# Kernel optimization log

Hardware: AMD Instinct MI355X
Metric: run time of the kernel (lower is better)

Reference implementation:

```python
import jax, jax.numpy as jnp
import numpy as np

N, E = 50000, 800000
H, C_HID = 4, 64  # heads, hidden_units
C_IN, C_OUT = 256, 64
NEG_SLOPE = 0.2
EPS = 1e-16


def gat_conv(x, src, dst, W, att_src, att_dst, bias):
    """PyG GATConv with concat=False (mean over heads) + bias.
    x: [N, F_in], W: [F_in, H*C], att_*: [H, C], bias: [C]."""
    n = x.shape[0]
    h = (x @ W).reshape(n, H, -1)                     # [N, H, C]
    a_src = jnp.sum(h * att_src, axis=-1)             # [N, H]
    a_dst = jnp.sum(h * att_dst, axis=-1)             # [N, H]
    e = jax.nn.leaky_relu(a_src[src] + a_dst[dst], NEG_SLOPE)  # [E, H]
    # segment softmax grouped by destination node
    m = jax.ops.segment_max(e, dst, num_segments=n)   # [N, H]
    e = jnp.exp(e - m[dst])
    denom = jax.ops.segment_sum(e, dst, num_segments=n)
    alpha = e / (denom[dst] + EPS)                    # [E, H]
    msg = h[src] * alpha[:, :, None]                  # [E, H, C]
    out = jax.ops.segment_sum(msg, dst, num_segments=n)  # [N, H, C]
    return out.mean(axis=1) + bias                    # concat=False -> head mean


def setup_inputs() -> dict:
    key = jax.random.key(0)
    ks = jax.random.split(key, 16)
    inp = {
        "x": jax.random.normal(ks[0], (N, C_IN), dtype=jnp.float32),
        "edge_index": jax.random.randint(ks[1], (2, E), 0, N, dtype=jnp.int64),
    }
    dims = [(C_IN, C_HID), (C_HID, C_HID), (C_HID, C_OUT)]
    for i, (fi, fo) in enumerate(dims, start=1):
        inp[f"W{i}"] = jax.random.normal(ks[2 + 4 * (i - 1)], (fi, H * fo), dtype=jnp.float32) * (1.0 / np.sqrt(fi))
        inp[f"as{i}"] = jax.random.normal(ks[3 + 4 * (i - 1)], (H, fo), dtype=jnp.float32) * 0.1
        inp[f"ad{i}"] = jax.random.normal(ks[4 + 4 * (i - 1)], (H, fo), dtype=jnp.float32) * 0.1
        inp[f"b{i}"] = jnp.zeros((fo,), dtype=jnp.float32)
    return inp


def reference(x, edge_index, W1, as1, ad1, b1, W2, as2, ad2, b2, W3, as3, ad3, b3):
    n = x.shape[0]
    loop = jnp.arange(n, dtype=edge_index.dtype)
    src = jnp.concatenate([edge_index[0], loop])  # add_self_loops=True (PyG default)
    dst = jnp.concatenate([edge_index[1], loop])
    layers = [(W1, as1, ad1, b1), (W2, as2, ad2, b2), (W3, as3, ad3, b3)]
    for (W, a_s, a_d, b) in layers:
        x = gat_conv(x, src, dst, W, a_s, a_d, b)
        x = jax.nn.relu(x)  # dropout is identity at inference
    return jax.nn.log_softmax(x, axis=-1)
```

## Files before the change

### kernel.cpp

```cpp
#include <hip/hip_runtime.h>
#include <hip/hip_bf16.h>
#include <math.h>
#include <stdint.h>

#define HEADS 4
#define CH 64
#define HC 256
#define NEG 0.2f
#define EPSV 1e-16f
#define NEGBIG -3.0e38f

typedef __attribute__((ext_vector_type(8))) short short8;
typedef __attribute__((ext_vector_type(4))) float f32x4;

__device__ __forceinline__ float lrelu(float x) { return x > 0.f ? x : NEG * x; }

__device__ __forceinline__ unsigned short f2bf(float f) {
  __hip_bfloat16 b = __float2bfloat16(f);
  return *reinterpret_cast<unsigned short*>(&b);
}
__device__ __forceinline__ float bf2f(unsigned short u) {
  return __uint_as_float((unsigned)u << 16);
}
__device__ __forceinline__ unsigned int packbf2(float a, float b) {
  return (unsigned int)f2bf(a) | ((unsigned int)f2bf(b) << 16);
}
__device__ __forceinline__ float unpack_lo(unsigned int v) {
  return __uint_as_float(v << 16);
}
__device__ __forceinline__ float unpack_hi(unsigned int v) {
  return __uint_as_float(v & 0xffff0000u);
}

__global__ __launch_bounds__(256) void wprep_k(const float* __restrict__ W,
                                               unsigned short* __restrict__ Wt,
                                               int K) {
  int i = blockIdx.x * 256 + threadIdx.x;
  if (i >= K * 256) return;
  int k = i >> 8, n = i & 255;
  Wt[(size_t)n * K + k] = f2bf(W[i]);
}

__global__ __launch_bounds__(256) void mfma_gat_k(const float* __restrict__ Af,
                                                  const unsigned short* __restrict__ Ab,
                                                  const unsigned short* __restrict__ Wt,
                                                  const float* __restrict__ att_s,
                                                  const float* __restrict__ att_d,
                                                  unsigned short* __restrict__ hb16,
                                                  float* __restrict__ a_src,
                                                  float* __restrict__ a_dst,
                                                  int M, int K, int a_is_f32) {
  __shared__ unsigned short As[32 * 40];
  __shared__ unsigned short Bs[256 * 40];
  __shared__ unsigned short Cs[32 * 258];

  int tid = threadIdx.x;
  int bm = blockIdx.x * 32;
  int w = tid >> 6, l = tid & 63;
  int lr = l & 15, lk = l >> 4;
  int row_s = tid >> 3, seg = tid & 7;

  f32x4 acc[2][4];
  #pragma unroll
  for (int rt = 0; rt < 2; ++rt)
    #pragma unroll
    for (int ct = 0; ct < 4; ++ct) {
      f32x4 z = {0.f, 0.f, 0.f, 0.f};
      acc[rt][ct] = z;
    }

  for (int k0 = 0; k0 < K; k0 += 32) {
    if (a_is_f32) {
      float4 v = make_float4(0.f, 0.f, 0.f, 0.f);
      if (bm + row_s < M)
        v = *reinterpret_cast<const float4*>(Af + (size_t)(bm + row_s) * K + k0 + seg * 4);
      ushort4 u;
      u.x = f2bf(v.x); u.y = f2bf(v.y); u.z = f2bf(v.z); u.w = f2bf(v.w);
      *reinterpret_cast<ushort4*>(&As[row_s * 40 + seg * 4]) = u;
    } else {
      ushort4 u = make_ushort4(0, 0, 0, 0);
      if (bm + row_s < M)
        u = *reinterpret_cast<const ushort4*>(Ab + (size_t)(bm + row_s) * K + k0 + seg * 4);
      *reinterpret_cast<ushort4*>(&As[row_s * 40 + seg * 4]) = u;
    }
    {
      const uint4* srcq = reinterpret_cast<const uint4*>(Wt + (size_t)tid * K + k0);
      uint4 q0 = srcq[0], q1 = srcq[1], q2 = srcq[2], q3 = srcq[3];
      uint4* dstq = reinterpret_cast<uint4*>(&Bs[tid * 40]);
      dstq[0] = q0; dstq[1] = q1; dstq[2] = q2; dstq[3] = q3;
    }
    __syncthreads();
    short8 bfr[4];
    #pragma unroll
    for (int ct = 0; ct < 4; ++ct)
      bfr[ct] = *reinterpret_cast<const short8*>(&Bs[(w * 64 + ct * 16 + lr) * 40 + lk * 8]);
    #pragma unroll
    for (int rt = 0; rt < 2; ++rt) {
      short8 af = *reinterpret_cast<const short8*>(&As[(rt * 16 + lr) * 40 + lk * 8]);
      #pragma unroll
      for (int ct = 0; ct < 4; ++ct)
        acc[rt][ct] = __builtin_amdgcn_mfma_f32_16x16x32_bf16(af, bfr[ct], acc[rt][ct], 0, 0, 0);
    }
    __syncthreads();
  }

  #pragma unroll
  for (int rt = 0; rt < 2; ++rt)
    #pragma unroll
    for (int ct = 0; ct < 4; ++ct)
      #pragma unroll
      for (int r = 0; r < 4; ++r) {
        int row = rt * 16 + lk * 4 + r;
        int c = ct * 16 + lr;
        Cs[row * 258 + c * 4 + w] = f2bf(acc[rt][ct][r]);
      }
  __syncthreads();

  if (bm + row_s < M) {
    ushort4* dst = reinterpret_cast<ushort4*>(hb16 + (size_t)(bm + row_s) * HC + seg * 32);
    const unsigned short* srcp = &Cs[row_s * 258 + seg * 32];
    #pragma unroll
    for (int q = 0; q < 4; ++q)
      dst[q] = *reinterpret_cast<const ushort4*>(srcp + q * 4);
  }

  {
    int nd = tid >> 3, q = tid & 7, h = q >> 1, half = q & 1;
    float ps = 0.f, pd = 0.f;
    const float* ats = att_s + h * 64 + half * 32;
    const float* atd = att_d + h * 64 + half * 32;
    const unsigned short* cp = &Cs[nd * 258 + (half * 32) * 4 + h];
    #pragma unroll
    for (int c = 0; c < 32; ++c) {
      float hv = bf2f(cp[c * 4]);
      ps += hv * ats[c];
      pd += hv * atd[c];
    }
    ps += __shfl_xor(ps, 1);
    pd += __shfl_xor(pd, 1);
    if (!(q & 1) && bm + nd < M) {
      a_src[(size_t)(bm + nd) * 4 + h] = ps;
      a_dst[(size_t)(bm + nd) * 4 + h] = pd;
    }
  }
}

__global__ __launch_bounds__(256) void zero2_k(int* __restrict__ a, int* __restrict__ b, int n) {
  int i = blockIdx.x * blockDim.x + threadIdx.x;
  if (i < n) { a[i] = 0; b[i] = 0; }
}

__global__ __launch_bounds__(256) void hist_k(const int* __restrict__ dst, int* __restrict__ count, int E) {
  int e = blockIdx.x * blockDim.x + threadIdx.x;
  if (e < E) atomicAdd(&count[dst[e]], 1);
}

__global__ __launch_bounds__(512) void scan1_k(const int* __restrict__ count,
                                               int* __restrict__ rp,
                                               int* __restrict__ bsum, int n) {
  __shared__ int sh[512];
  int tx = threadIdx.x;
  int i = blockIdx.x * 512 + tx;
  int v = (i < n) ? count[i] : 0;
  sh[tx] = v;
  __syncthreads();
  #pragma unroll
  for (int off = 1; off < 512; off <<= 1) {
    int t = (tx >= off) ? sh[tx - off] : 0;
    __syncthreads();
    sh[tx] += t;
    __syncthreads();
  }
  if (i < n) rp[i] = sh[tx] - v;
  if (tx == 511) bsum[blockIdx.x] = sh[511];
}

__global__ __launch_bounds__(128) void scan2_k(int* __restrict__ bsum, int nb) {
  __shared__ int sh[128];
  int tx = threadIdx.x;
  int v = (tx < nb) ? bsum[tx] : 0;
  sh[tx] = v;
  __syncthreads();
  #pragma unroll
  for (int off = 1; off < 128; off <<= 1) {
    int t = (tx >= off) ? sh[tx - off] : 0;
    __syncthreads();
    sh[tx] += t;
    __syncthreads();
  }
  if (tx < nb) bsum[tx] = sh[tx] - v;
}

__global__ __launch_bounds__(512) void scan3_k(int* __restrict__ rp, const int* __restrict__ bsum,
                                               int n, int E) {
  int i = blockIdx.x * 512 + threadIdx.x;
  if (i < n) rp[i] += bsum[blockIdx.x];
  if (i == 0) rp[n] = E;
}

__global__ __launch_bounds__(256) void scatter_k(const int* __restrict__ src, const int* __restrict__ dst,
                                                 const int* __restrict__ rp, int* __restrict__ cursor,
                                                 int* __restrict__ csr_src, int E) {
  int e = blockIdx.x * blockDim.x + threadIdx.x;
  if (e >= E) return;
  int d = dst[e];
  int pos = rp[d] + atomicAdd(&cursor[d], 1);
  csr_src[pos] = src[e];
}

__global__ __launch_bounds__(256) void soft_agg_k(const int* __restrict__ rp,
                                                  const int* __restrict__ csr_src,
                                                  const float* __restrict__ a_src,
                                                  const float* __restrict__ a_dst,
                                                  const unsigned short* __restrict__ hb16,
                                                  const float* __restrict__ bias,
                                                  float* __restrict__ outf,
                                                  unsigned short* __restrict__ outb,
                                                  int N, int do_lsm) {
  __shared__ uint4 rec[4][64];
  int tid  = threadIdx.x;
  int w    = tid >> 6;
  int lane = tid & 63;
  int wid  = (blockIdx.x * blockDim.x + tid) >> 6;
  if (wid >= N) return;
  int rs = rp[wid], re = rp[wid + 1];

  float4 ad4 = *reinterpret_cast<const float4*>(a_dst + (size_t)wid * 4);
  float4 asn = *reinterpret_cast<const float4*>(a_src + (size_t)wid * 4);
  float es0 = lrelu(asn.x + ad4.x), es1 = lrelu(asn.y + ad4.y);
  float es2 = lrelu(asn.z + ad4.z), es3 = lrelu(asn.w + ad4.w);

  int sreg = 0;
  float e0 = NEGBIG, e1 = NEGBIG, e2 = NEGBIG, e3 = NEGBIG;
  if (rs + lane < re) {
    sreg = csr_src[rs + lane];
    float4 a = *reinterpret_cast<const float4*>(a_src + (size_t)sreg * 4);
    e0 = lrelu(a.x + ad4.x); e1 = lrelu(a.y + ad4.y);
    e2 = lrelu(a.z + ad4.z); e3 = lrelu(a.w + ad4.w);
  }
  float m0 = fmaxf(es0, e0), m1 = fmaxf(es1, e1);
  float m2 = fmaxf(es2, e2), m3 = fmaxf(es3, e3);
  for (int base = rs + 64; base < re; base += 64) {
    if (base + lane < re) {
      int s = csr_src[base + lane];
      float4 a = *reinterpret_cast<const float4*>(a_src + (size_t)s * 4);
      m0 = fmaxf(m0, lrelu(a.x + ad4.x)); m1 = fmaxf(m1, lrelu(a.y + ad4.y));
      m2 = fmaxf(m2, lrelu(a.z + ad4.z)); m3 = fmaxf(m3, lrelu(a.w + ad4.w));
    }
  }
  #pragma unroll
  for (int off = 32; off > 0; off >>= 1) {
    m0 = fmaxf(m0, __shfl_xor(m0, off));
    m1 = fmaxf(m1, __shfl_xor(m1, off));
    m2 = fmaxf(m2, __shfl_xor(m2, off));
    m3 = fmaxf(m3, __shfl_xor(m3, off));
  }

  float a0 = 0.f, a1 = 0.f, a2 = 0.f, a3 = 0.f;
  float dn0 = 0.f, dn1 = 0.f, dn2 = 0.f, dn3 = 0.f;
  uint4* recw = &rec[w][0];
  const unsigned short* hl = hb16 + lane * 4;

  auto agg_lds = [&](int cnt) {
    int k = 0;
    for (; k + 4 <= cnt; k += 4) {
      uint4 r0 = recw[k + 0], r1 = recw[k + 1], r2 = recw[k + 2], r3 = recw[k + 3];
      ushort4 h0 = *reinterpret_cast<const ushort4*>(hl + (size_t)r0.x * HC);
      ushort4 h1 = *reinterpret_cast<const ushort4*>(hl + (size_t)r1.x * HC);
      ushort4 h2 = *reinterpret_cast<const ushort4*>(hl + (size_t)r2.x * HC);
      ushort4 h3 = *reinterpret_cast<const ushort4*>(hl + (size_t)r3.x * HC);
      a0 += unpack_lo(r0.y) * bf2f(h0.x) + unpack_lo(r1.y) * bf2f(h1.x)
          + unpack_lo(r2.y) * bf2f(h2.x) + unpack_lo(r3.y) * bf2f(h3.x);
      a1 += unpack_hi(r0.y) * bf2f(h0.y) + unpack_hi(r1.y) * bf2f(h1.y)
          + unpack_hi(r2.y) * bf2f(h2.y) + unpack_hi(r3.y) * bf2f(h3.y);
      a2 += unpack_lo(r0.z) * bf2f(h0.z) + unpack_lo(r1.z) * bf2f(h1.z)
          + unpack_lo(r2.z) * bf2f(h2.z) + unpack_lo(r3.z) * bf2f(h3.z);
      a3 += unpack_hi(r0.z) * bf2f(h0.w) + unpack_hi(r1.z) * bf2f(h1.w)
          + unpack_hi(r2.z) * bf2f(h2.w) + unpack_hi(r3.z) * bf2f(h3.w);
    }
    for (; k < cnt; ++k) {
      uint4 r0 = recw[k];
      ushort4 hv = *reinterpret_cast<const ushort4*>(hl + (size_t)r0.x * HC);
      a0 += unpack_lo(r0.y) * bf2f(hv.x);
      a1 += unpack_hi(r0.y) * bf2f(hv.y);
      a2 += unpack_lo(r0.z) * bf2f(hv.z);
      a3 += unpack_hi(r0.z) * bf2f(hv.w);
    }
  };

  {
    float px = expf(e0 - m0), py = expf(e1 - m1);
    float pz = expf(e2 - m2), pw = expf(e3 - m3);
    dn0 += px; dn1 += py; dn2 += pz; dn3 += pw;
    recw[lane] = make_uint4((unsigned)sreg, packbf2(px, py), packbf2(pz, pw), 0u);
    int cnt = re - rs; if (cnt > 64) cnt = 64;
    agg_lds(cnt);
  }
  for (int base = rs + 64; base < re; base += 64) {
    int s = 0;
    float f0 = NEGBIG, f1 = NEGBIG, f2 = NEGBIG, f3 = NEGBIG;
    if (base + lane < re) {
      s = csr_src[base + lane];
      float4 a = *reinterpret_cast<const float4*>(a_src + (size_t)s * 4);
      f0 = lrelu(a.x + ad4.x); f1 = lrelu(a.y + ad4.y);
      f2 = lrelu(a.z + ad4.z); f3 = lrelu(a.w + ad4.w);
    }
    float px = expf(f0 - m0), py = expf(f1 - m1);
    float pz = expf(f2 - m2), pw = expf(f3 - m3);
    dn0 += px; dn1 += py; dn2 += pz; dn3 += pw;
    recw[lane] = make_uint4((unsigned)s, packbf2(px, py), packbf2(pz, pw), 0u);
    int cnt = re - base; if (cnt > 64) cnt = 64;
    agg_lds(cnt);
  }

  #pragma unroll
  for (int off = 32; off > 0; off >>= 1) {
    dn0 += __shfl_xor(dn0, off);
    dn1 += __shfl_xor(dn1, off);
    dn2 += __shfl_xor(dn2, off);
    dn3 += __shfl_xor(dn3, off);
  }
  float sp0 = expf(es0 - m0), sp1 = expf(es1 - m1);
  float sp2 = expf(es2 - m2), sp3 = expf(es3 - m3);
  dn0 += sp0; dn1 += sp1; dn2 += sp2; dn3 += sp3;
  float r0 = 1.f / (dn0 + EPSV), r1 = 1.f / (dn1 + EPSV);
  float r2 = 1.f / (dn2 + EPSV), r3 = 1.f / (dn3 + EPSV);

  ushort4 sh = *reinterpret_cast<const ushort4*>(hb16 + (size_t)wid * HC + lane * 4);
  float sum = (a0 + sp0 * bf2f(sh.x)) * r0
            + (a1 + sp1 * bf2f(sh.y)) * r1
            + (a2 + sp2 * bf2f(sh.z)) * r2
            + (a3 + sp3 * bf2f(sh.w)) * r3;
  float v = sum * 0.25f + bias[lane];
  v = fmaxf(v, 0.f);
  if (do_lsm) {
    float mx = v;
    #pragma unroll
    for (int off = 32; off > 0; off >>= 1) mx = fmaxf(mx, __shfl_xor(mx, off));
    float ex = expf(v - mx);
    float sm = ex;
    #pragma unroll
    for (int off = 32; off > 0; off >>= 1) sm += __shfl_xor(sm, off);
    outf[(size_t)wid * CH + lane] = v - mx - logf(sm);
  } else {
    outb[(size_t)wid * CH + lane] = f2bf(v);
  }
}

extern "C" void kernel_launch(void* const* d_in, const int* in_sizes, int n_in,
                              void* d_out, int out_size, void* d_ws, size_t ws_size,
                              hipStream_t stream) {
  const float* x0 = (const float*)d_in[0];
  const int*   ei = (const int*)d_in[1];
  int N = in_sizes[0] / HC;
  int E = in_sizes[1] / 2;
  const int* srcp = ei;
  const int* dstp = ei + E;

  const float* W[3]  = {(const float*)d_in[2], (const float*)d_in[6],  (const float*)d_in[10]};
  const float* AS[3] = {(const float*)d_in[3], (const float*)d_in[7],  (const float*)d_in[11]};
  const float* AD[3] = {(const float*)d_in[4], (const float*)d_in[8],  (const float*)d_in[12]};
  const float* BI[3] = {(const float*)d_in[5], (const float*)d_in[9],  (const float*)d_in[13]};
  int Kdim[3] = {256, 64, 64};

  char* ws = (char*)d_ws;
  size_t off = 0;
  auto alloc = [&](size_t bytes) {
    void* p = ws + off;
    off += (bytes + 255) & ~(size_t)255;
    return p;
  };
  unsigned short* hb16    = (unsigned short*)alloc((size_t)N * HC * 2);
  unsigned short* xb16    = (unsigned short*)alloc((size_t)N * CH * 2);
  float*          a_s     = (float*)alloc((size_t)N * 4 * 4);
  float*          a_d     = (float*)alloc((size_t)N * 4 * 4);
  int*            rowp    = (int*)alloc((size_t)(N + 1) * 4);
  int*            cursor  = (int*)alloc((size_t)N * 4);
  int*            csr_src = (int*)alloc((size_t)E * 4);
  int*            bsum    = (int*)alloc(512 * 4);
  unsigned short* Wt[3];
  Wt[0] = (unsigned short*)alloc((size_t)256 * 256 * 2);
  Wt[1] = (unsigned short*)alloc((size_t)256 * 64 * 2);
  Wt[2] = (unsigned short*)alloc((size_t)256 * 64 * 2);

  for (int L = 0; L < 3; ++L) {
    int tot = Kdim[L] * 256;
    wprep_k<<<(tot + 255) / 256, 256, 0, stream>>>(W[L], Wt[L], Kdim[L]);
  }

  int nb = (N + 511) / 512;
  zero2_k<<<(N + 255) / 256, 256, 0, stream>>>(cursor, rowp, N);
  hist_k<<<(E + 255) / 256, 256, 0, stream>>>(dstp, rowp, E);
  scan1_k<<<nb, 512, 0, stream>>>(rowp, rowp, bsum, N);
  scan2_k<<<1, 128, 0, stream>>>(bsum, nb);
  scan3_k<<<nb, 512, 0, stream>>>(rowp, bsum, N, E);
  scatter_k<<<(E + 255) / 256, 256, 0, stream>>>(srcp, dstp, rowp, cursor, csr_src, E);

  for (int L = 0; L < 3; ++L) {
    int K = Kdim[L];
    mfma_gat_k<<<(N + 31) / 32, 256, 0, stream>>>(
        (L == 0) ? x0 : nullptr, (L == 0) ? nullptr : xb16,
        Wt[L], AS[L], AD[L], hb16, a_s, a_d, N, K, (L == 0) ? 1 : 0);
    soft_agg_k<<<(N + 3) / 4, 256, 0, stream>>>(rowp, csr_src, a_s, a_d, hb16, BI[L],
                                                (float*)d_out, xb16, N, (L == 2) ? 1 : 0);
  }
}
```

Baseline: 402.1 us.

## Store features as fp16 and aggregate with pre-normalized alphas via fdot2

Switches the stored node features from bf16 to fp16. Attention weights are normalized before aggregation by adding an extra pass that computes the softmax denominator. The per-edge accumulation collapses the four head accumulators into one, using packed fp16 dot2 instructions that do the head-mean reduction directly. readfirstlane on the gathered source index makes the address wave-uniform. The cost is an extra pass over the neighbor list and a_src per node, plus fp16 range and precision risk.

New measurement: 391.8 us. -2.6%, faster.

```diff
diff --git a/kernel.cpp b/kernel.cpp
--- a/kernel.cpp
+++ b/kernel.cpp
@@ -12,6 +12,8 @@
 
 typedef __attribute__((ext_vector_type(8))) short short8;
 typedef __attribute__((ext_vector_type(4))) float f32x4;
+typedef _Float16 f16_t;
+typedef __fp16 fp16x2 __attribute__((ext_vector_type(2)));
 
 __device__ __forceinline__ float lrelu(float x) { return x > 0.f ? x : NEG * x; }
 
@@ -22,14 +24,19 @@
 __device__ __forceinline__ float bf2f(unsigned short u) {
   return __uint_as_float((unsigned)u << 16);
 }
-__device__ __forceinline__ unsigned int packbf2(float a, float b) {
-  return (unsigned int)f2bf(a) | ((unsigned int)f2bf(b) << 16);
-}
-__device__ __forceinline__ float unpack_lo(unsigned int v) {
-  return __uint_as_float(v << 16);
-}
-__device__ __forceinline__ float unpack_hi(unsigned int v) {
-  return __uint_as_float(v & 0xffff0000u);
+__device__ __forceinline__ unsigned int pkf16(float a, float b) {
+  fp16x2 v = __builtin_amdgcn_cvt_pkrtz(a, b);
+  return __builtin_bit_cast(unsigned int, v);
+}
+__device__ __forceinline__ float dot2acc(unsigned int a, unsigned int h, float acc) {
+#if __has_builtin(__builtin_amdgcn_fdot2)
+  return __builtin_amdgcn_fdot2(__builtin_bit_cast(fp16x2, a),
+                                __builtin_bit_cast(fp16x2, h), acc, false);
+#else
+  fp16x2 av = __builtin_bit_cast(fp16x2, a);
+  fp16x2 hv = __builtin_bit_cast(fp16x2, h);
+  return acc + (float)av[0] * (float)hv[0] + (float)av[1] * (float)hv[1];
+#endif
 }
 
 __global__ __launch_bounds__(256) void wprep_k(const float* __restrict__ W,
@@ -46,7 +53,7 @@
                                                   const unsigned short* __restrict__ Wt,
                                                   const float* __restrict__ att_s,
                                                   const float* __restrict__ att_d,
-                                                  unsigned short* __restrict__ hb16,
+                                                  unsigned short* __restrict__ ht16,
                                                   float* __restrict__ a_src,
                                                   float* __restrict__ a_dst,
                                                   int M, int K, int a_is_f32) {
@@ -112,12 +119,12 @@
       for (int r = 0; r < 4; ++r) {
         int row = rt * 16 + lk * 4 + r;
         int c = ct * 16 + lr;
-        Cs[row * 258 + c * 4 + w] = f2bf(acc[rt][ct][r]);
+        Cs[row * 258 + c * 4 + w] = __builtin_bit_cast(unsigned short, (f16_t)acc[rt][ct][r]);
       }
   __syncthreads();
 
   if (bm + row_s < M) {
-    ushort4* dst = reinterpret_cast<ushort4*>(hb16 + (size_t)(bm + row_s) * HC + seg * 32);
+    ushort4* dst = reinterpret_cast<ushort4*>(ht16 + (size_t)(bm + row_s) * HC + seg * 32);
     const unsigned short* srcp = &Cs[row_s * 258 + seg * 32];
     #pragma unroll
     for (int q = 0; q < 4; ++q)
@@ -132,7 +139,7 @@
     const unsigned short* cp = &Cs[nd * 258 + (half * 32) * 4 + h];
     #pragma unroll
     for (int c = 0; c < 32; ++c) {
-      float hv = bf2f(cp[c * 4]);
+      float hv = (float)__builtin_bit_cast(f16_t, cp[c * 4]);
       ps += hv * ats[c];
       pd += hv * atd[c];
     }
@@ -212,7 +219,7 @@
                                                   const int* __restrict__ csr_src,
                                                   const float* __restrict__ a_src,
                                                   const float* __restrict__ a_dst,
-                                                  const unsigned short* __restrict__ hb16,
+                                                  const unsigned short* __restrict__ ht16,
                                                   const float* __restrict__ bias,
                                                   float* __restrict__ outf,
                                                   unsigned short* __restrict__ outb,
@@ -256,43 +263,63 @@
     m3 = fmaxf(m3, __shfl_xor(m3, off));
   }
 
-  float a0 = 0.f, a1 = 0.f, a2 = 0.f, a3 = 0.f;
-  float dn0 = 0.f, dn1 = 0.f, dn2 = 0.f, dn3 = 0.f;
+  float px = expf(e0 - m0), py = expf(e1 - m1);
+  float pz = expf(e2 - m2), pw = expf(e3 - m3);
+  float dn0 = px, dn1 = py, dn2 = pz, dn3 = pw;
+  for (int base = rs + 64; base < re; base += 64) {
+    if (base + lane < re) {
+      int s = csr_src[base + lane];
+      float4 a = *reinterpret_cast<const float4*>(a_src + (size_t)s * 4);
+      dn0 += expf(lrelu(a.x + ad4.x) - m0); dn1 += expf(lrelu(a.y + ad4.y) - m1);
+      dn2 += expf(lrelu(a.z + ad4.z) - m2); dn3 += expf(lrelu(a.w + ad4.w) - m3);
+    }
+  }
+  #pragma unroll
+  for (int off = 32; off > 0; off >>= 1) {
+    dn0 += __shfl_xor(dn0, off);
+    dn1 += __shfl_xor(dn1, off);
+    dn2 += __shfl_xor(dn2, off);
+    dn3 += __shfl_xor(dn3, off);
+  }
+  float sp0 = expf(es0 - m0), sp1 = expf(es1 - m1);
+  float sp2 = expf(es2 - m2), sp3 = expf(es3 - m3);
+  dn0 += sp0; dn1 += sp1; dn2 += sp2; dn3 += sp3;
+  float rr0 = 1.f / (dn0 + EPSV), rr1 = 1.f / (dn1 + EPSV);
+  float rr2 = 1.f / (dn2 + EPSV), rr3 = 1.f / (dn3 + EPSV);
+
+  float acc = 0.f;
   uint4* recw = &rec[w][0];
-  const unsigned short* hl = hb16 + lane * 4;
+  const unsigned short* hl = ht16 + lane * 4;
 
   auto agg_lds = [&](int cnt) {
     int k = 0;
     for (; k + 4 <= cnt; k += 4) {
       uint4 r0 = recw[k + 0], r1 = recw[k + 1], r2 = recw[k + 2], r3 = recw[k + 3];
-      ushort4 h0 = *reinterpret_cast<const ushort4*>(hl + (size_t)r0.x * HC);
-      ushort4 h1 = *reinterpret_cast<const ushort4*>(hl + (size_t)r1.x * HC);
-      ushort4 h2 = *reinterpret_cast<const ushort4*>(hl + (size_t)r2.x * HC);
-      ushort4 h3 = *reinterpret_cast<const ushort4*>(hl + (size_t)r3.x * HC);
-      a0 += unpack_lo(r0.y) * bf2f(h0.x) + unpack_lo(r1.y) * bf2f(h1.x)
-          + unpack_lo(r2.y) * bf2f(h2.x) + unpack_lo(r3.y) * bf2f(h3.x);
-      a1 += unpack_hi(r0.y) * bf2f(h0.y) + unpack_hi(r1.y) * bf2f(h1.y)
-          + unpack_hi(r2.y) * bf2f(h2.y) + unpack_hi(r3.y) * bf2f(h3.y);
-      a2 += unpack_lo(r0.z) * bf2f(h0.z) + unpack_lo(r1.z) * bf2f(h1.z)
-          + unpack_lo(r2.z) * bf2f(h2.z) + unpack_lo(r3.z) * bf2f(h3.z);
-      a3 += unpack_hi(r0.z) * bf2f(h0.w) + unpack_hi(r1.z) * bf2f(h1.w)
-          + unpack_hi(r2.z) * bf2f(h2.w) + unpack_hi(r3.z) * bf2f(h3.w);
+      int s0 = __builtin_amdgcn_readfirstlane((int)r0.x);
+      int s1 = __builtin_amdgcn_readfirstlane((int)r1.x);
+      int s2 = __builtin_amdgcn_readfirstlane((int)r2.x);
+      int s3 = __builtin_amdgcn_readfirstlane((int)r3.x);
+      uint2 h0 = *reinterpret_cast<const uint2*>(hl + (size_t)s0 * HC);
+      uint2 h1 = *reinterpret_cast<const uint2*>(hl + (size_t)s1 * HC);
+      uint2 h2 = *reinterpret_cast<const uint2*>(hl + (size_t)s2 * HC);
+      uint2 h3 = *reinterpret_cast<const uint2*>(hl + (size_t)s3 * HC);
+      acc = dot2acc(r0.y, h0.x, acc); acc = dot2acc(r0.z, h0.y, acc);
+      acc = dot2acc(r1.y, h1.x, acc); acc = dot2acc(r1.z, h1.y, acc);
+      acc = dot2acc(r2.y, h2.x, acc); acc = dot2acc(r2.z, h2.y, acc);
+      acc = dot2acc(r3.y, h3.x, acc); acc = dot2acc(r3.z, h3.y, acc);
     }
     for (; k < cnt; ++k) {
       uint4 r0 = recw[k];
-      ushort4 hv = *reinterpret_cast<const ushort4*>(hl + (size_t)r0.x * HC);
-      a0 += unpack_lo(r0.y) * bf2f(hv.x);
-      a1 += unpack_hi(r0.y) * bf2f(hv.y);
-      a2 += unpack_lo(r0.z) * bf2f(hv.z);
-      a3 += unpack_hi(r0.z) * bf2f(hv.w);
+      int s0 = __builtin_amdgcn_readfirstlane((int)r0.x);
+      uint2 hv = *reinterpret_cast<const uint2*>(hl + (size_t)s0 * HC);
+      acc = dot2acc(r0.y, hv.x, acc);
+      acc = dot2acc(r0.z, hv.y, acc);
     }
   };
 
   {
-    float px = expf(e0 - m0), py = expf(e1 - m1);
-    float pz = expf(e2 - m2), pw = expf(e3 - m3);
-    dn0 += px; dn1 += py; dn2 += pz; dn3 += pw;
-    recw[lane] = make_uint4((unsigned)sreg, packbf2(px, py), packbf2(pz, pw), 0u);
+    recw[lane] = make_uint4((unsigned)sreg, pkf16(px * rr0, py * rr1),
+                            pkf16(pz * rr2, pw * rr3), 0u);
     int cnt = re - rs; if (cnt > 64) cnt = 64;
     agg_lds(cnt);
   }
@@ -305,33 +332,17 @@
       f0 = lrelu(a.x + ad4.x); f1 = lrelu(a.y + ad4.y);
       f2 = lrelu(a.z + ad4.z); f3 = lrelu(a.w + ad4.w);
     }
-    float px = expf(f0 - m0), py = expf(f1 - m1);
-    float pz = expf(f2 - m2), pw = expf(f3 - m3);
-    dn0 += px; dn1 += py; dn2 += pz; dn3 += pw;
-    recw[lane] = make_uint4((unsigned)s, packbf2(px, py), packbf2(pz, pw), 0u);
+    float qx = expf(f0 - m0) * rr0, qy = expf(f1 - m1) * rr1;
+    float qz = expf(f2 - m2) * rr2, qw = expf(f3 - m3) * rr3;
+    recw[lane] = make_uint4((unsigned)s, pkf16(qx, qy), pkf16(qz, qw), 0u);
     int cnt = re - base; if (cnt > 64) cnt = 64;
     agg_lds(cnt);
   }
 
-  #pragma unroll
-  for (int off = 32; off > 0; off >>= 1) {
-    dn0 += __shfl_xor(dn0, off);
-    dn1 += __shfl_xor(dn1, off);
-    dn2 += __shfl_xor(dn2, off);
-    dn3 += __shfl_xor(dn3, off);
-  }
-  float sp0 = expf(es0 - m0), sp1 = expf(es1 - m1);
-  float sp2 = expf(es2 - m2), sp3 = expf(es3 - m3);
-  dn0 += sp0; dn1 += sp1; dn2 += sp2; dn3 += sp3;
-  float r0 = 1.f / (dn0 + EPSV), r1 = 1.f / (dn1 + EPSV);
-  float r2 = 1.f / (dn2 + EPSV), r3 = 1.f / (dn3 + EPSV);
-
-  ushort4 sh = *reinterpret_cast<const ushort4*>(hb16 + (size_t)wid * HC + lane * 4);
-  float sum = (a0 + sp0 * bf2f(sh.x)) * r0
-            + (a1 + sp1 * bf2f(sh.y)) * r1
-            + (a2 + sp2 * bf2f(sh.z)) * r2
-            + (a3 + sp3 * bf2f(sh.w)) * r3;
-  float v = sum * 0.25f + bias[lane];
+  uint2 shv = *reinterpret_cast<const uint2*>(ht16 + (size_t)wid * HC + lane * 4);
+  acc = dot2acc(pkf16(sp0 * rr0, sp1 * rr1), shv.x, acc);
+  acc = dot2acc(pkf16(sp2 * rr2, sp3 * rr3), shv.y, acc);
+  float v = acc * 0.25f + bias[lane];
   v = fmaxf(v, 0.f);
   if (do_lsm) {
     float mx = v;
@@ -370,7 +381,7 @@
     off += (bytes + 255) & ~(size_t)255;
     return p;
   };
-  unsigned short* hb16    = (unsigned short*)alloc((size_t)N * HC * 2);
+  unsigned short* ht16    = (unsigned short*)alloc((size_t)N * HC * 2);
   unsigned short* xb16    = (unsigned short*)alloc((size_t)N * CH * 2);
   float*          a_s     = (float*)alloc((size_t)N * 4 * 4);
   float*          a_d     = (float*)alloc((size_t)N * 4 * 4);
@@ -400,8 +411,8 @@
     int K = Kdim[L];
     mfma_gat_k<<<(N + 31) / 32, 256, 0, stream>>>(
         (L == 0) ? x0 : nullptr, (L == 0) ? nullptr : xb16,
-        Wt[L], AS[L], AD[L], hb16, a_s, a_d, N, K, (L == 0) ? 1 : 0);
-    soft_agg_k<<<(N + 3) / 4, 256, 0, stream>>>(rowp, csr_src, a_s, a_d, hb16, BI[L],
+        Wt[L], AS[L], AD[L], ht16, a_s, a_d, N, K, (L == 0) ? 1 : 0);
+    soft_agg_k<<<(N + 3) / 4, 256, 0, stream>>>(rowp, csr_src, a_s, a_d, ht16, BI[L],
                                                 (float*)d_out, xb16, N, (L == 2) ? 1 : 0);
   }
 }
```
